# Performance work log

Hardware: AMD Instinct MI355X
Metric: run time of the kernel (lower is better)

The kernel has to match this reference:

```python
import jax, jax.numpy as jnp
import numpy as np

LORA_ALPHA = 16.0
TOP_K = 2


def setup_inputs() -> dict:
    key = jax.random.key(0)
    k_x, k_w, k_g, k_a, k_b = jax.random.split(key, 5)
    B, S, H, O, E, R = 2, 2048, 2048, 2048, 8, 16
    x = jax.random.normal(k_x, (B, S, H), dtype=jnp.float32)
    weight = jax.random.normal(k_w, (O, H), dtype=jnp.float32)          # frozen base W [out, in]
    gate_w = jax.random.normal(k_g, (E, H), dtype=jnp.float32) * 0.02   # router gate [E, in]
    A_w = jax.random.normal(k_a, (E, R, H), dtype=jnp.float32) * (1.0 / np.sqrt(H))  # stacked lora_A
    B_w = jax.random.normal(k_b, (E, O, R), dtype=jnp.float32) * 0.01   # stacked lora_B
    return {"x": x, "weight": weight, "gate_w": gate_w, "A_w": A_w, "B_w": B_w}


def reference(x, weight, gate_w, A_w, B_w):
    E = gate_w.shape[0]
    # Base frozen linear: F.linear(x, weight)
    out = jnp.einsum("bsh,oh->bso", x, weight)

    # Router: softmax over experts, top-2, renormalize
    logits = jnp.einsum("bsh,eh->bse", x, gate_w)
    probs = jax.nn.softmax(logits, axis=-1)
    topk_w, topk_idx = jax.lax.top_k(probs, TOP_K)          # [b,s,2]
    topk_w = topk_w / jnp.sum(topk_w, axis=-1, keepdims=True)

    # Per-token combine weight for each expert (sum over the 2 slots)
    onehot = jax.nn.one_hot(topk_idx, E, dtype=x.dtype)      # [b,s,2,E]
    cw = jnp.einsum("bsk,bske->bse", topk_w, onehot)         # [b,s,E]

    # LoRA: down-project into all experts' rank spaces, weight, then up-project.
    # t: [b,s,E,r] is small (r=16); weighting here avoids a [b,s,E,out] buffer.
    t = jnp.einsum("bsh,erh->bser", x, A_w)
    t = t * cw[..., None]
    lora = jnp.einsum("bser,eor->bso", t, B_w)

    return out + LORA_ALPHA * lora
```

## Files before the change

### kernel.cpp

```cpp
#include <hip/hip_runtime.h>
#include <hip/hip_bf16.h>


typedef __bf16 bf16x8 __attribute__((ext_vector_type(8)));
typedef float f32x4 __attribute__((ext_vector_type(4)));

__device__ __forceinline__ __bf16 f2bf(float f) {
  union { float f; unsigned u; } v; v.f = f;
  unsigned r = (v.u + 0x7FFFu + ((v.u >> 16) & 1u)) >> 16;
  unsigned short s = (unsigned short)r;
  return __builtin_bit_cast(__bf16, s);
}

__device__ __forceinline__ void ld_lds16(const void* g, void* l) {
  __builtin_amdgcn_global_load_lds((__attribute__((address_space(1))) void*)g,
                                   (__attribute__((address_space(3))) void*)l,
                                   16, 0, 0);
}

__global__ void prep_kernel(const float* __restrict__ W, const float* __restrict__ Aw,
                            const float* __restrict__ Bw, __bf16* __restrict__ Bfull,
                            __bf16* __restrict__ A2) {
  const int b = blockIdx.x, tid = threadIdx.x;
  if (b < 2176) {
    const float* src = (b < 2048) ? (W + (size_t)b * 2048)
                                  : (Aw + (size_t)(b - 2048) * 2048);
    __bf16* dst = (b < 2048) ? (Bfull + (size_t)b * 2176)
                             : (A2 + (size_t)(b - 2048) * 2048);
    const int c = tid * 8;
    float4 a = *(const float4*)(src + c);
    float4 d = *(const float4*)(src + c + 4);
    bf16x8 v;
    v[0] = f2bf(a.x); v[1] = f2bf(a.y); v[2] = f2bf(a.z); v[3] = f2bf(a.w);
    v[4] = f2bf(d.x); v[5] = f2bf(d.y); v[6] = f2bf(d.z); v[7] = f2bf(d.w);
    *(bf16x8*)(dst + c) = v;
  } else {
    const int idx = (b - 2176) * 256 + tid;
    const int e = idx >> 11, o = idx & 2047;
    const float4* s = (const float4*)(Bw + ((size_t)e * 2048 + o) * 16);
    float4 v0 = s[0], v1 = s[1], v2 = s[2], v3 = s[3];
    __bf16* d = Bfull + (size_t)o * 2176 + 2048 + e * 16;
    bf16x8 lo, hi;
    lo[0] = f2bf(v0.x); lo[1] = f2bf(v0.y); lo[2] = f2bf(v0.z); lo[3] = f2bf(v0.w);
    lo[4] = f2bf(v1.x); lo[5] = f2bf(v1.y); lo[6] = f2bf(v1.z); lo[7] = f2bf(v1.w);
    hi[0] = f2bf(v2.x); hi[1] = f2bf(v2.y); hi[2] = f2bf(v2.z); hi[3] = f2bf(v2.w);
    hi[4] = f2bf(v3.x); hi[5] = f2bf(v3.y); hi[6] = f2bf(v3.z); hi[7] = f2bf(v3.w);
    *(bf16x8*)d = lo;
    *(bf16x8*)(d + 8) = hi;
  }
}

__global__ __launch_bounds__(256) void conv_router(
    const float* __restrict__ x, const float* __restrict__ gw,
    __bf16* __restrict__ Abuf, float* __restrict__ cw) {
  __shared__ float red[256][17];
  __shared__ float red2[16][17];
  const int tid = threadIdx.x;
  const int t0 = blockIdx.x * 2;
  const int c = tid * 8;

  float4 a0 = *(const float4*)(x + (size_t)t0 * 2048 + c);
  float4 b0 = *(const float4*)(x + (size_t)t0 * 2048 + c + 4);
  float4 a1 = *(const float4*)(x + (size_t)(t0 + 1) * 2048 + c);
  float4 b1 = *(const float4*)(x + (size_t)(t0 + 1) * 2048 + c + 4);
  float xf0[8] = {a0.x, a0.y, a0.z, a0.w, b0.x, b0.y, b0.z, b0.w};
  float xf1[8] = {a1.x, a1.y, a1.z, a1.w, b1.x, b1.y, b1.z, b1.w};

  bf16x8 v0, v1;
#pragma unroll
  for (int j = 0; j < 8; ++j) { v0[j] = f2bf(xf0[j]); v1[j] = f2bf(xf1[j]); }
  *(bf16x8*)(Abuf + (size_t)t0 * 2176 + c) = v0;
  *(bf16x8*)(Abuf + (size_t)(t0 + 1) * 2176 + c) = v1;

  float acc0[8], acc1[8];
#pragma unroll
  for (int e = 0; e < 8; ++e) { acc0[e] = 0.0f; acc1[e] = 0.0f; }
#pragma unroll
  for (int e = 0; e < 8; ++e) {
    float4 g0 = *(const float4*)(gw + e * 2048 + c);
    float4 g1 = *(const float4*)(gw + e * 2048 + c + 4);
    float gg[8] = {g0.x, g0.y, g0.z, g0.w, g1.x, g1.y, g1.z, g1.w};
#pragma unroll
    for (int j = 0; j < 8; ++j) {
      acc0[e] += xf0[j] * gg[j];
      acc1[e] += xf1[j] * gg[j];
    }
  }
#pragma unroll
  for (int e = 0; e < 8; ++e) { red[tid][e] = acc0[e]; red[tid][8 + e] = acc1[e]; }
  __syncthreads();
  {
    const int p = tid & 15, ch = tid >> 4;
    float s = 0.0f;
#pragma unroll
    for (int i = 0; i < 16; ++i) s += red[ch * 16 + i][p];
    red2[ch][p] = s;
  }
  __syncthreads();
  if (tid < 2) {
    float lg[8];
#pragma unroll
    for (int e = 0; e < 8; ++e) {
      float s = 0.0f;
#pragma unroll
      for (int ch = 0; ch < 16; ++ch) s += red2[ch][tid * 8 + e];
      lg[e] = s;
    }
    int a = 0;
    for (int e = 1; e < 8; ++e) if (lg[e] > lg[a]) a = e;
    int b = (a == 0) ? 1 : 0;
    for (int e = 0; e < 8; ++e) if (e != a && lg[e] > lg[b]) b = e;
    const float d = __expf(lg[b] - lg[a]);
    float o[8] = {0, 0, 0, 0, 0, 0, 0, 0};
    o[a] = 1.0f / (1.0f + d);
    o[b] = d / (1.0f + d);
    const int t = t0 + tid;
#pragma unroll
    for (int e = 0; e < 8; ++e) cw[t * 8 + e] = o[e];
  }
}

__global__ __launch_bounds__(256) void t2_scale(
    const __bf16* __restrict__ Abuf_x, const __bf16* __restrict__ A2,
    const float* __restrict__ cw, __bf16* __restrict__ Abuf) {
  const int tid = threadIdx.x;
  const int wave = tid >> 6, lane = tid & 63;
  const int t0 = blockIdx.x * 16;
  const int jg = blockIdx.y * 4 + wave;
  const int m = lane & 15, q = lane >> 4;

  const __bf16* arow = Abuf_x + (size_t)(t0 + m) * 2176 + q * 8;
  const __bf16* brow = A2 + (size_t)(jg * 16 + m) * 2048 + q * 8;
  f32x4 acc0 = {}, acc1 = {};
  for (int ks = 0; ks < 64; ks += 2) {
    bf16x8 af0 = *(const bf16x8*)(arow + ks * 32);
    bf16x8 bf0 = *(const bf16x8*)(brow + ks * 32);
    bf16x8 af1 = *(const bf16x8*)(arow + ks * 32 + 32);
    bf16x8 bf1 = *(const bf16x8*)(brow + ks * 32 + 32);
    acc0 = __builtin_amdgcn_mfma_f32_16x16x32_bf16(af0, bf0, acc0, 0, 0, 0);
    acc1 = __builtin_amdgcn_mfma_f32_16x16x32_bf16(af1, bf1, acc1, 0, 0, 0);
  }
#pragma unroll
  for (int rg = 0; rg < 4; ++rg) {
    const int t = t0 + q * 4 + rg;
    const float s = (acc0[rg] + acc1[rg]) * 16.0f * cw[t * 8 + jg];
    Abuf[(size_t)t * 2176 + 2048 + jg * 16 + m] = f2bf(s);
  }
}

__global__ __launch_bounds__(256, 4) void mfma_gemm_bt(
    const __bf16* __restrict__ A, const __bf16* __restrict__ B,
    float* __restrict__ C, int lda, int ldb, int ldc, int kiters) {
  __shared__ __align__(16) __bf16 As[128 * 64];
  __shared__ __align__(16) __bf16 Bs[64 * 64];
  const int tid = threadIdx.x;
  const int wave = tid >> 6;
  const int lane = tid & 63;
  const int tm = blockIdx.x * 128;
  const int tn = blockIdx.y * 64;

  const int wm = (wave >> 1) * 64;
  const int wn = (wave & 1) * 32;
  const int srow = lane >> 3;
  const int skoff = ((lane & 7) ^ srow) * 8;

  const int rlo = lane & 7;
  const int rb3 = (lane >> 3) & 1;
  const int qb = lane >> 4;

  f32x4 acc[4][2] = {};

  int kcur = 0;
  for (int kt = 0; kt < kiters; ++kt) {
#pragma unroll
    for (int r = 0; r < 4; ++r) {
      const int ch = r * 4 + wave;
      ld_lds16(A + (size_t)(tm + ch * 8 + srow) * lda + kcur + skoff, &As[ch * 512]);
    }
#pragma unroll
    for (int r = 0; r < 2; ++r) {
      const int ch = r * 4 + wave;
      ld_lds16(B + (size_t)(tn + ch * 8 + srow) * ldb + kcur + skoff, &Bs[ch * 512]);
    }
    __syncthreads();
#pragma unroll
    for (int ks = 0; ks < 2; ++ks) {
      bf16x8 af[4], bfg[2];
      const int q8 = ((ks * 4 + qb) ^ rlo) * 8;
#pragma unroll
      for (int i = 0; i < 4; ++i) {
        const int rh = ((wm + i * 16) >> 3) + rb3;
        af[i] = *(const bf16x8*)&As[rh * 512 + rlo * 64 + q8];
      }
#pragma unroll
      for (int j = 0; j < 2; ++j) {
        const int rh = ((wn + j * 16) >> 3) + rb3;
        bfg[j] = *(const bf16x8*)&Bs[rh * 512 + rlo * 64 + q8];
      }
#pragma unroll
      for (int i = 0; i < 4; ++i)
#pragma unroll
        for (int j = 0; j < 2; ++j)
          acc[i][j] = __builtin_amdgcn_mfma_f32_16x16x32_bf16(af[i], bfg[j], acc[i][j], 0, 0, 0);
    }
    __syncthreads();
    kcur += 64;
  }

  const int crow0 = tm + wm + (lane >> 4) * 4;
  const int ccol0 = tn + wn + (lane & 15);
#pragma unroll
  for (int i = 0; i < 4; ++i)
#pragma unroll
    for (int j = 0; j < 2; ++j)
#pragma unroll
      for (int rg = 0; rg < 4; ++rg)
        C[(size_t)(crow0 + i * 16 + rg) * ldc + ccol0 + j * 16] = acc[i][j][rg];
}

extern "C" void kernel_launch(void* const* d_in, const int* in_sizes, int n_in,
                              void* d_out, int out_size, void* d_ws, size_t ws_size,
                              hipStream_t stream) {
  const float* x = (const float*)d_in[0];
  const float* weight = (const float*)d_in[1];
  const float* gate_w = (const float*)d_in[2];
  const float* A_w = (const float*)d_in[3];
  const float* B_w = (const float*)d_in[4];
  float* out = (float*)d_out;

  char* ws = (char*)d_ws;
  __bf16* Abuf = (__bf16*)ws;
  __bf16* Bfull = (__bf16*)(ws + 17825792);
  __bf16* A2 = (__bf16*)(ws + 26738688);
  float* cw = (float*)(ws + 27262976);

  prep_kernel<<<2240, 256, 0, stream>>>(weight, A_w, B_w, Bfull, A2);
  conv_router<<<2048, 256, 0, stream>>>(x, gate_w, Abuf, cw);
  t2_scale<<<dim3(256, 2), 256, 0, stream>>>(Abuf, A2, cw, Abuf);
  mfma_gemm_bt<<<dim3(32, 32), 256, 0, stream>>>(Abuf, Bfull, out, 2176, 2176,
                                                 2048, 34);
}
```

Measured before the change: 181.6 us.

## Merge prep and router kernels, split-K t2_scale, enlarge GEMM tile to 128x128

```diff
diff --git a/kernel.cpp b/kernel.cpp
--- a/kernel.cpp
+++ b/kernel.cpp
@@ -18,9 +18,12 @@
                                    16, 0, 0);
 }
 
-__global__ void prep_kernel(const float* __restrict__ W, const float* __restrict__ Aw,
-                            const float* __restrict__ Bw, __bf16* __restrict__ Bfull,
-                            __bf16* __restrict__ A2) {
+__global__ __launch_bounds__(256) void setup_kernel(
+    const float* __restrict__ W, const float* __restrict__ Aw,
+    const float* __restrict__ Bw, const float* __restrict__ x,
+    const float* __restrict__ gw, __bf16* __restrict__ Bfull,
+    __bf16* __restrict__ A2, __bf16* __restrict__ Abuf,
+    float* __restrict__ cw) {
   const int b = blockIdx.x, tid = threadIdx.x;
   if (b < 2176) {
     const float* src = (b < 2048) ? (W + (size_t)b * 2048)
@@ -34,7 +37,9 @@
     v[0] = f2bf(a.x); v[1] = f2bf(a.y); v[2] = f2bf(a.z); v[3] = f2bf(a.w);
     v[4] = f2bf(d.x); v[5] = f2bf(d.y); v[6] = f2bf(d.z); v[7] = f2bf(d.w);
     *(bf16x8*)(dst + c) = v;
-  } else {
+    return;
+  }
+  if (b < 2240) {
     const int idx = (b - 2176) * 256 + tid;
     const int e = idx >> 11, o = idx & 2047;
     const float4* s = (const float4*)(Bw + ((size_t)e * 2048 + o) * 16);
@@ -47,16 +52,11 @@
     hi[4] = f2bf(v3.x); hi[5] = f2bf(v3.y); hi[6] = f2bf(v3.z); hi[7] = f2bf(v3.w);
     *(bf16x8*)d = lo;
     *(bf16x8*)(d + 8) = hi;
-  }
-}
-
-__global__ __launch_bounds__(256) void conv_router(
-    const float* __restrict__ x, const float* __restrict__ gw,
-    __bf16* __restrict__ Abuf, float* __restrict__ cw) {
+    return;
+  }
   __shared__ float red[256][17];
   __shared__ float red2[16][17];
-  const int tid = threadIdx.x;
-  const int t0 = blockIdx.x * 2;
+  const int t0 = (b - 2240) * 2;
   const int c = tid * 8;
 
   float4 a0 = *(const float4*)(x + (size_t)t0 * 2048 + c);
@@ -108,12 +108,12 @@
     }
     int a = 0;
     for (int e = 1; e < 8; ++e) if (lg[e] > lg[a]) a = e;
-    int b = (a == 0) ? 1 : 0;
-    for (int e = 0; e < 8; ++e) if (e != a && lg[e] > lg[b]) b = e;
-    const float d = __expf(lg[b] - lg[a]);
+    int bb = (a == 0) ? 1 : 0;
+    for (int e = 0; e < 8; ++e) if (e != a && lg[e] > lg[bb]) bb = e;
+    const float d = __expf(lg[bb] - lg[a]);
     float o[8] = {0, 0, 0, 0, 0, 0, 0, 0};
     o[a] = 1.0f / (1.0f + d);
-    o[b] = d / (1.0f + d);
+    o[bb] = d / (1.0f + d);
     const int t = t0 + tid;
 #pragma unroll
     for (int e = 0; e < 8; ++e) cw[t * 8 + e] = o[e];
@@ -123,16 +123,18 @@
 __global__ __launch_bounds__(256) void t2_scale(
     const __bf16* __restrict__ Abuf_x, const __bf16* __restrict__ A2,
     const float* __restrict__ cw, __bf16* __restrict__ Abuf) {
+  __shared__ f32x4 part[4][64];
   const int tid = threadIdx.x;
   const int wave = tid >> 6, lane = tid & 63;
   const int t0 = blockIdx.x * 16;
-  const int jg = blockIdx.y * 4 + wave;
+  const int e = blockIdx.y;
   const int m = lane & 15, q = lane >> 4;
 
-  const __bf16* arow = Abuf_x + (size_t)(t0 + m) * 2176 + q * 8;
-  const __bf16* brow = A2 + (size_t)(jg * 16 + m) * 2048 + q * 8;
+  const __bf16* arow = Abuf_x + (size_t)(t0 + m) * 2176 + wave * 512 + q * 8;
+  const __bf16* brow = A2 + (size_t)(e * 16 + m) * 2048 + wave * 512 + q * 8;
   f32x4 acc0 = {}, acc1 = {};
-  for (int ks = 0; ks < 64; ks += 2) {
+#pragma unroll
+  for (int ks = 0; ks < 16; ks += 2) {
     bf16x8 af0 = *(const bf16x8*)(arow + ks * 32);
     bf16x8 bf0 = *(const bf16x8*)(brow + ks * 32);
     bf16x8 af1 = *(const bf16x8*)(arow + ks * 32 + 32);
@@ -140,27 +142,32 @@
     acc0 = __builtin_amdgcn_mfma_f32_16x16x32_bf16(af0, bf0, acc0, 0, 0, 0);
     acc1 = __builtin_amdgcn_mfma_f32_16x16x32_bf16(af1, bf1, acc1, 0, 0, 0);
   }
-#pragma unroll
-  for (int rg = 0; rg < 4; ++rg) {
-    const int t = t0 + q * 4 + rg;
-    const float s = (acc0[rg] + acc1[rg]) * 16.0f * cw[t * 8 + jg];
-    Abuf[(size_t)t * 2176 + 2048 + jg * 16 + m] = f2bf(s);
-  }
-}
-
-__global__ __launch_bounds__(256, 4) void mfma_gemm_bt(
+  part[wave][lane] = acc0 + acc1;
+  __syncthreads();
+  if (wave == 0) {
+    f32x4 s = part[0][lane] + part[1][lane] + part[2][lane] + part[3][lane];
+#pragma unroll
+    for (int rg = 0; rg < 4; ++rg) {
+      const int t = t0 + q * 4 + rg;
+      Abuf[(size_t)t * 2176 + 2048 + e * 16 + m] =
+          f2bf(s[rg] * 16.0f * cw[t * 8 + e]);
+    }
+  }
+}
+
+__global__ __launch_bounds__(512, 4) void mfma_gemm_bt(
     const __bf16* __restrict__ A, const __bf16* __restrict__ B,
     float* __restrict__ C, int lda, int ldb, int ldc, int kiters) {
   __shared__ __align__(16) __bf16 As[128 * 64];
-  __shared__ __align__(16) __bf16 Bs[64 * 64];
+  __shared__ __align__(16) __bf16 Bs[128 * 64];
   const int tid = threadIdx.x;
   const int wave = tid >> 6;
   const int lane = tid & 63;
   const int tm = blockIdx.x * 128;
-  const int tn = blockIdx.y * 64;
-
-  const int wm = (wave >> 1) * 64;
-  const int wn = (wave & 1) * 32;
+  const int tn = blockIdx.y * 128;
+
+  const int wm = (wave >> 2) * 64;
+  const int wn = (wave & 3) * 32;
   const int srow = lane >> 3;
   const int skoff = ((lane & 7) ^ srow) * 8;
 
@@ -173,13 +180,9 @@
   int kcur = 0;
   for (int kt = 0; kt < kiters; ++kt) {
 #pragma unroll
-    for (int r = 0; r < 4; ++r) {
-      const int ch = r * 4 + wave;
+    for (int r = 0; r < 2; ++r) {
+      const int ch = r * 8 + wave;
       ld_lds16(A + (size_t)(tm + ch * 8 + srow) * lda + kcur + skoff, &As[ch * 512]);
-    }
-#pragma unroll
-    for (int r = 0; r < 2; ++r) {
-      const int ch = r * 4 + wave;
       ld_lds16(B + (size_t)(tn + ch * 8 + srow) * ldb + kcur + skoff, &Bs[ch * 512]);
     }
     __syncthreads();
@@ -234,9 +237,9 @@
   __bf16* A2 = (__bf16*)(ws + 26738688);
   float* cw = (float*)(ws + 27262976);
 
-  prep_kernel<<<2240, 256, 0, stream>>>(weight, A_w, B_w, Bfull, A2);
-  conv_router<<<2048, 256, 0, stream>>>(x, gate_w, Abuf, cw);
-  t2_scale<<<dim3(256, 2), 256, 0, stream>>>(Abuf, A2, cw, Abuf);
-  mfma_gemm_bt<<<dim3(32, 32), 256, 0, stream>>>(Abuf, Bfull, out, 2176, 2176,
+  setup_kernel<<<4288, 256, 0, stream>>>(weight, A_w, B_w, x, gate_w, Bfull, A2,
+                                         Abuf, cw);
+  t2_scale<<<dim3(256, 8), 256, 0, stream>>>(Abuf, A2, cw, Abuf);
+  mfma_gemm_bt<<<dim3(32, 16), 512, 0, stream>>>(Abuf, Bfull, out, 2176, 2176,
                                                  2048, 34);
 }
```

After: 175.1 us, median of 2. -3.6%, faster.
